# Kernel optimization log

Hardware: AMD Instinct MI355X
Metric: run time of the kernel (lower is better)

The kernel has to match this reference:

```python
import jax, jax.numpy as jnp
import numpy as np

B = 512
N_DRUGS = 4096
H_DRUG = 1023          # per-drug feature dim; input to MLP is 2*(H_DRUG+1) = 2048
N_CELL = 32
DIMS = [2048, 2048, 1024, 512, 1]


def setup_inputs() -> dict:
    key = jax.random.key(0)
    ks = jax.random.split(key, 12)
    pairs = jax.random.randint(ks[0], (B, 2), 0, N_DRUGS)
    cell_lines = jax.random.randint(ks[1], (B,), 0, N_CELL)
    attrs = jax.random.normal(ks[2], (B, 4), dtype=jnp.float32)
    h_drug = jax.random.normal(ks[3], (N_DRUGS, H_DRUG), dtype=jnp.float32)
    # shared Linear layers (torch Linear: y = x @ W.T + b), kaiming-uniform-ish init
    def lin(k, fan_in, fan_out):
        k1, k2 = jax.random.split(k)
        bound = 1.0 / np.sqrt(fan_in)
        W = jax.random.uniform(k1, (fan_out, fan_in), jnp.float32, -bound, bound)
        b = jax.random.uniform(k2, (fan_out,), jnp.float32, -bound, bound)
        return W, b
    W0, b0 = lin(ks[4], DIMS[0], DIMS[1])
    W1, b1 = lin(ks[5], DIMS[1], DIMS[2])
    # cell-line specific layers: 1/100 * randn
    L0 = 0.01 * jax.random.normal(ks[6], (N_CELL, DIMS[3], DIMS[2]), dtype=jnp.float32)
    O0 = 0.01 * jax.random.normal(ks[7], (N_CELL, DIMS[3], 1), dtype=jnp.float32)
    L1 = 0.01 * jax.random.normal(ks[8], (N_CELL, DIMS[4], DIMS[3]), dtype=jnp.float32)
    O1 = 0.01 * jax.random.normal(ks[9], (N_CELL, DIMS[4], 1), dtype=jnp.float32)
    return {"pairs": pairs, "cell_lines": cell_lines, "attrs": attrs, "h_drug": h_drug,
            "W0": W0, "b0": b0, "W1": W1, "b1": b1,
            "L0": L0, "O0": O0, "L1": L1, "O1": O1}


def reference(pairs, cell_lines, attrs, h_drug, W0, b0, W1, b1, L0, O0, L1, O1):
    n_attr = attrs.shape[1] // 2
    h1 = h_drug[pairs[:, 0]]                               # [B, H_DRUG]
    h2 = h_drug[pairs[:, 1]]
    bd1 = jnp.concatenate([h1, attrs[:, n_attr - 1:n_attr]], axis=1)
    bd2 = jnp.concatenate([h2, attrs[:, -1:]], axis=1)
    # original flips order with p=0.5 (data augmentation); fixed to (bd1, bd2) for determinism
    x = jnp.concatenate([bd1, bd2], axis=1)                # [B, 2048]
    # shared MLP (note: original applies relu(relu(x)) == relu(x))
    x = jax.nn.relu(x @ W0.T + b0)                         # [B, 2048]
    x = jax.nn.relu(x @ W1.T + b1)                         # [B, 1024]
    # cell-line-specific layers: gather per-sample weight and batched matvec
    x = jax.nn.relu(jnp.einsum('boi,bi->bo', L0[cell_lines], x) + O0[cell_lines, :, 0])  # [B, 512]
    x = jnp.einsum('boi,bi->bo', L1[cell_lines], x) + O1[cell_lines, :, 0]               # [B, 1]
    return x[:, 0]
```

## Files before the change

kernel.cpp:

```cpp
#include <hip/hip_runtime.h>

typedef short s16x8 __attribute__((ext_vector_type(8)));
typedef float f32x4 __attribute__((ext_vector_type(4)));
typedef unsigned short u16;

#define BATCH 512
#define HD    1023
#define K0    2048
#define N0    2048
#define N1    1024
#define N2    512

__device__ __forceinline__ u16 f2bf(float f) {
  unsigned u = __builtin_bit_cast(unsigned, f);
  unsigned r = (u + 0x7fffu + ((u >> 16) & 1u)) >> 16;
  return (u16)r;
}

__device__ __forceinline__ s16x8 pack8(f32x4 a, f32x4 b) {
  union { unsigned u[4]; s16x8 v; } r;
  asm("v_cvt_pk_bf16_f32 %0, %1, %2" : "=v"(r.u[0]) : "v"(a[0]), "v"(a[1]));
  asm("v_cvt_pk_bf16_f32 %0, %1, %2" : "=v"(r.u[1]) : "v"(a[2]), "v"(a[3]));
  asm("v_cvt_pk_bf16_f32 %0, %1, %2" : "=v"(r.u[2]) : "v"(b[0]), "v"(b[1]));
  asm("v_cvt_pk_bf16_f32 %0, %1, %2" : "=v"(r.u[3]) : "v"(b[2]), "v"(b[3]));
  return r.v;
}

__global__ __launch_bounds__(256) void k_prep(
    const int* __restrict__ pairs, const float* __restrict__ attrs,
    const float* __restrict__ h_drug, const float* __restrict__ W0,
    const float* __restrict__ W1, const int* __restrict__ cells,
    const float* __restrict__ O1, u16* __restrict__ xb,
    u16* __restrict__ w0b, u16* __restrict__ w1b, float* __restrict__ out) {
  const int bid = blockIdx.x, tid = threadIdx.x;
  if (bid < 512) {
    const int b = bid;
    const float* h0 = h_drug + (size_t)pairs[2 * b] * HD;
    const float* h1 = h_drug + (size_t)pairs[2 * b + 1] * HD;
    u16* xr = xb + (size_t)b * K0;
    for (int i = tid; i < HD; i += 256) {
      xr[i] = f2bf(h0[i]);
      xr[1024 + i] = f2bf(h1[i]);
    }
    if (tid == 0) {
      xr[1023] = f2bf(attrs[4 * b + 1]);
      xr[2047] = f2bf(attrs[4 * b + 3]);
      out[b] = O1[cells[b]];
    }
  } else if (bid < 1536) {
    const size_t e = ((size_t)(bid - 512) * 256 + tid) * 16;
    f32x4 a = *(const f32x4*)(W0 + e),     b2 = *(const f32x4*)(W0 + e + 4);
    f32x4 c = *(const f32x4*)(W0 + e + 8), d  = *(const f32x4*)(W0 + e + 12);
    *(s16x8*)(w0b + e)     = pack8(a, b2);
    *(s16x8*)(w0b + e + 8) = pack8(c, d);
  } else {
    const size_t e = ((size_t)(bid - 1536) * 256 + tid) * 16;
    f32x4 a = *(const f32x4*)(W1 + e),     b2 = *(const f32x4*)(W1 + e + 4);
    f32x4 c = *(const f32x4*)(W1 + e + 8), d  = *(const f32x4*)(W1 + e + 12);
    *(s16x8*)(w1b + e)     = pack8(a, b2);
    *(s16x8*)(w1b + e + 8) = pack8(c, d);
  }
}

#define GI(s, t) { \
  pa0_##s = *(const s16x8*)(agp0 + (size_t)(t) * 128); \
  if constexpr (AF == 2) pa1_##s = *(const s16x8*)(agp1 + (size_t)(t) * 128); \
  pb_##s = *(const s16x8*)(bgp0 + (size_t)(t) * 128); }

#define GS(s, t, DOLOAD) { \
  char* buf = lds[(s) & 1]; \
  *(s16x8*)(buf + awo0) = pa0_##s; \
  if constexpr (AF == 2) *(s16x8*)(buf + awo1) = pa1_##s; \
  *(s16x8*)(buf + ABYTES + bwo0) = pb_##s; \
  asm volatile("s_waitcnt lgkmcnt(0)" ::: "memory"); \
  __builtin_amdgcn_s_barrier(); \
  asm volatile("" ::: "memory"); \
  if (DOLOAD) GI(s, (t) + 4) \
  __builtin_amdgcn_s_setprio(1); \
  _Pragma("unroll") \
  for (int ks = 0; ks < 2; ++ks) { \
    const int kq = ((ks << 6) | lk) ^ sw; \
    s16x8 a0 = *(const s16x8*)(buf + aoff + kq); \
    s16x8 b0 = *(const s16x8*)(buf + ABYTES + boff + kq); \
    acc0 = __builtin_amdgcn_mfma_f32_16x16x32_bf16(a0, b0, acc0, 0, 0, 0); \
    if constexpr (AF == 2) { \
      s16x8 a1 = *(const s16x8*)(buf + aoff + 2048 + kq); \
      acc1 = __builtin_amdgcn_mfma_f32_16x16x32_bf16(a1, b0, acc1, 0, 0, 0); \
    } \
  } \
  __builtin_amdgcn_s_setprio(0); }

template <int BM, int N>
__global__ __launch_bounds__(256) void k_gemm(
    const u16* __restrict__ A, const u16* __restrict__ B,
    const float* __restrict__ bias, u16* __restrict__ Y) {
  constexpr int K = 2048;
  constexpr int AF = BM / 32;
  constexpr int ABYTES = BM * 128;
  constexpr int NBMSH = (BM == 64) ? 3 : 4;
  __shared__ char lds[2][ABYTES + 4096];
  const int tid = threadIdx.x;
  const int w = tid >> 6, l = tid & 63;
  const int wr = w >> 1, wc = w & 1;
  const int lrow = l & 15;
  const int lk = (l >> 4) << 4;
  const int sw = (lrow & 7) << 4;

  const int wgid = (blockIdx.x & 7) * 64 + (blockIdx.x >> 3);
  const int bn = wgid >> NBMSH, bm = wgid & ((1 << NBMSH) - 1);

  const size_t K2 = (size_t)K * 2;
  const char* Ag = (const char*)A + (size_t)bm * BM * K2;
  const char* Bg = (const char*)B + (size_t)(bn * 32) * K2;

  const int o0 = tid * 16;
  const int ar0 = o0 >> 7, ac0 = o0 & 127;
  const char* agp0 = Ag + (size_t)ar0 * K2 + ac0;
  const int awo0 = (ar0 << 7) + (ac0 ^ ((ar0 & 7) << 4));
  const int o1 = o0 + 4096;
  const int ar1 = o1 >> 7, ac1 = o1 & 127;
  const char* agp1 = Ag + (size_t)ar1 * K2 + ac1;
  const int awo1 = (ar1 << 7) + (ac1 ^ ((ar1 & 7) << 4));

  const char* bgp0 = Bg + (size_t)ar0 * K2 + ac0;
  const int bwo0 = awo0;

  const int aoff = (wr * (BM / 2) + lrow) * 128;
  const int boff = (wc * 16 + lrow) * 128;

  f32x4 acc0 = {}, acc1 = {};
  s16x8 pa0_0, pa0_1, pa0_2, pa0_3;
  s16x8 pa1_0, pa1_1, pa1_2, pa1_3;
  s16x8 pb_0, pb_1, pb_2, pb_3;

  GI(0, 0) GI(1, 1) GI(2, 2) GI(3, 3)
  constexpr int NT = 32;
  int t = 0;
  for (; t < NT - 4; t += 4) {
    GS(0, t, 1) GS(1, t + 1, 1) GS(2, t + 2, 1) GS(3, t + 3, 1)
  }
  GS(0, t, 0) GS(1, t + 1, 0) GS(2, t + 2, 0) GS(3, t + 3, 0)

  const int colg = bn * 32 + wc * 16 + lrow;
  const int rowb = bm * BM + wr * (BM / 2) + ((l >> 4) << 2);
  const float bv = bias[colg];
#pragma unroll
  for (int fa = 0; fa < AF; ++fa)
#pragma unroll
    for (int r = 0; r < 4; ++r) {
      float v = (fa ? acc1 : acc0)[r] + bv;
      v = v > 0.f ? v : 0.f;
      Y[(size_t)(rowb + fa * 16 + r) * N + colg] = f2bf(v);
    }
}

#define H_ISSUE(S, ch) { \
  const float* src = hsrc + (ch) * 256; \
  q0_##S = *(const f32x4*)(src);      q1_##S = *(const f32x4*)(src + 4); \
  q2_##S = *(const f32x4*)(src + 8);  q3_##S = *(const f32x4*)(src + 12); \
  q4_##S = *(const f32x4*)(src + 16); q5_##S = *(const f32x4*)(src + 20); \
  q6_##S = *(const f32x4*)(src + 24); q7_##S = *(const f32x4*)(src + 28); }

#define H_WRITE(S, ch) { \
  char* dst = lbuf[(ch) & 1] + (hrow << 9); \
  *(s16x8*)(dst + ((hcb + 0)  ^ hswz)) = pack8(q0_##S, q1_##S); \
  *(s16x8*)(dst + ((hcb + 16) ^ hswz)) = pack8(q2_##S, q3_##S); \
  *(s16x8*)(dst + ((hcb + 32) ^ hswz)) = pack8(q4_##S, q5_##S); \
  *(s16x8*)(dst + ((hcb + 48) ^ hswz)) = pack8(q6_##S, q7_##S); }

#define H_SYNC { \
  asm volatile("s_waitcnt lgkmcnt(0)" ::: "memory"); \
  __builtin_amdgcn_s_barrier(); \
  asm volatile("" ::: "memory"); }

#define H_MFMA(ch) { \
  const char* bb = lbuf[(ch) & 1]; \
  s16x8 bv0 = *(const s16x8*)(bb + ((0 * 16 + lrow) << 9) + kboff); \
  s16x8 bv1 = *(const s16x8*)(bb + ((1 * 16 + lrow) << 9) + kboff); \
  s16x8 bv2 = *(const s16x8*)(bb + ((2 * 16 + lrow) << 9) + kboff); \
  s16x8 bv3 = *(const s16x8*)(bb + ((3 * 16 + lrow) << 9) + kboff); \
  s16x8 av0 = *(const s16x8*)(ap0 + (ch) * 256); \
  s16x8 av1 = *(const s16x8*)(ap1 + (ch) * 256); \
  __builtin_amdgcn_s_setprio(1); \
  acc[0][0] = __builtin_amdgcn_mfma_f32_16x16x32_bf16(av0, bv0, acc[0][0], 0, 0, 0); \
  acc[0][1] = __builtin_amdgcn_mfma_f32_16x16x32_bf16(av0, bv1, acc[0][1], 0, 0, 0); \
  acc[0][2] = __builtin_amdgcn_mfma_f32_16x16x32_bf16(av0, bv2, acc[0][2], 0, 0, 0); \
  acc[0][3] = __builtin_amdgcn_mfma_f32_16x16x32_bf16(av0, bv3, acc[0][3], 0, 0, 0); \
  acc[1][0] = __builtin_amdgcn_mfma_f32_16x16x32_bf16(av1, bv0, acc[1][0], 0, 0, 0); \
  acc[1][1] = __builtin_amdgcn_mfma_f32_16x16x32_bf16(av1, bv1, acc[1][1], 0, 0, 0); \
  acc[1][2] = __builtin_amdgcn_mfma_f32_16x16x32_bf16(av1, bv2, acc[1][2], 0, 0, 0); \
  acc[1][3] = __builtin_amdgcn_mfma_f32_16x16x32_bf16(av1, bv3, acc[1][3], 0, 0, 0); \
  __builtin_amdgcn_s_setprio(0); }

__global__ __launch_bounds__(512) void k_head(
    const int* __restrict__ cells, const u16* __restrict__ y2b,
    const float* __restrict__ L0, const float* __restrict__ O0,
    const float* __restrict__ L1, float* __restrict__ out) {
  __shared__ int slist[544];
  __shared__ int scnt;
  __shared__ float red[8][2048];
  __shared__ char lbuf[2][32768];
  const int tid = threadIdx.x;
  const int c = blockIdx.x >> 3, rt = blockIdx.x & 7;
  if (tid == 0) scnt = 0;
  __syncthreads();
  for (int i = tid; i < BATCH; i += 512)
    if (cells[i] == c) slist[atomicAdd(&scnt, 1)] = i;
  __syncthreads();
  const int ns = scnt;
  if (ns == 0) return;
  const int npad = (ns + 31) & ~31;
  for (int i = ns + tid; i < npad; i += 512) slist[i] = slist[0];
  __syncthreads();

  const int w = tid >> 6, l = tid & 63;
  const int lrow = l & 15;
  const int r0 = rt * 64;
  const float* L0c = L0 + ((size_t)c * N2 + r0) * N1;
  const int hrow = tid >> 3;
  const int hcb = (tid & 7) * 64;
  const int hswz = (hrow & 7) << 4;
  const float* hsrc = L0c + (size_t)hrow * N1 + (tid & 7) * 32;
  const int kboff = ((w * 64 + ((l >> 4) << 4)) ^ ((lrow & 7) << 4));

  f32x4 q0_A, q1_A, q2_A, q3_A, q4_A, q5_A, q6_A, q7_A;
  f32x4 q0_B, q1_B, q2_B, q3_B, q4_B, q5_B, q6_B, q7_B;

  for (int cb = 0; cb < npad; cb += 32) {
    const u16* ap0 = y2b + (size_t)slist[cb + lrow] * N1 + w * 32 + ((l >> 4) << 3);
    const u16* ap1 = y2b + (size_t)slist[cb + 16 + lrow] * N1 + w * 32 + ((l >> 4) << 3);
    f32x4 acc[2][4] = {};
    H_ISSUE(A, 0)
    H_WRITE(A, 0)
    H_ISSUE(B, 1)
    H_SYNC
    H_MFMA(0)
    H_WRITE(B, 1)
    H_ISSUE(A, 2)
    H_SYNC
    H_MFMA(1)
    H_WRITE(A, 2)
    H_ISSUE(B, 3)
    H_SYNC
    H_MFMA(2)
    H_WRITE(B, 3)
    H_SYNC
    H_MFMA(3)

    __syncthreads();
#pragma unroll
    for (int h = 0; h < 2; ++h)
#pragma unroll
      for (int fb = 0; fb < 4; ++fb)
#pragma unroll
        for (int r = 0; r < 4; ++r) {
          const int s0 = h * 16 + (l >> 4) * 4 + r;
          red[w][s0 * 64 + fb * 16 + lrow] = acc[h][fb][r];
        }
    __syncthreads();
    {
      const int s = tid >> 4;
      const int rq = (tid & 15) * 4;
      if (cb + s < ns) {
        float p = 0.f;
#pragma unroll
        for (int j = 0; j < 4; ++j) {
          const int r = rq + j, e = s * 64 + r;
          float v = red[0][e] + red[1][e] + red[2][e] + red[3][e] +
                    red[4][e] + red[5][e] + red[6][e] + red[7][e] +
                    O0[(size_t)c * N2 + r0 + r];
          v = v > 0.f ? v : 0.f;
          p += v * L1[(size_t)c * N2 + r0 + r];
        }
#pragma unroll
        for (int off = 8; off; off >>= 1) p += __shfl_xor(p, off, 16);
        if ((tid & 15) == 0) atomicAdd(&out[slist[cb + s]], p);
      }
    }
  }
}

extern "C" void kernel_launch(void* const* d_in, const int* in_sizes, int n_in,
                              void* d_out, int out_size, void* d_ws, size_t ws_size,
                              hipStream_t stream) {
  const int*   pairs  = (const int*)d_in[0];
  const int*   cells  = (const int*)d_in[1];
  const float* attrs  = (const float*)d_in[2];
  const float* h_drug = (const float*)d_in[3];
  const float* W0     = (const float*)d_in[4];
  const float* b0     = (const float*)d_in[5];
  const float* W1     = (const float*)d_in[6];
  const float* b1     = (const float*)d_in[7];
  const float* L0     = (const float*)d_in[8];
  const float* O0     = (const float*)d_in[9];
  const float* L1     = (const float*)d_in[10];
  const float* O1     = (const float*)d_in[11];
  float* out = (float*)d_out;

  char* ws = (char*)d_ws;
  u16* xb  = (u16*)(ws);
  u16* w0b = (u16*)(ws + (2u  << 20));
  u16* w1b = (u16*)(ws + (10u << 20));
  u16* y1b = (u16*)(ws + (14u << 20));
  u16* y2b = (u16*)(ws + (16u << 20));

  k_prep<<<2048, 256, 0, stream>>>(pairs, attrs, h_drug, W0, W1, cells, O1,
                                   xb, w0b, w1b, out);
  k_gemm<64, N0><<<512, 256, 0, stream>>>(xb, w0b, b0, y1b);
  k_gemm<32, N1><<<512, 256, 0, stream>>>(y1b, w1b, b1, y2b);
  k_head<<<256, 512, 0, stream>>>(cells, y2b, L0, O0, L1, out);
}
```

Measured before the change: 48.26 us.

## Move W1 bf16 conversion into first GEMM launch and enlarge its tiles

New measurement: 46.22 us. 4.2% less time.

```diff
diff --git a/kernel.cpp b/kernel.cpp
--- a/kernel.cpp
+++ b/kernel.cpp
@@ -29,9 +29,8 @@
 __global__ __launch_bounds__(256) void k_prep(
     const int* __restrict__ pairs, const float* __restrict__ attrs,
     const float* __restrict__ h_drug, const float* __restrict__ W0,
-    const float* __restrict__ W1, const int* __restrict__ cells,
-    const float* __restrict__ O1, u16* __restrict__ xb,
-    u16* __restrict__ w0b, u16* __restrict__ w1b, float* __restrict__ out) {
+    const int* __restrict__ cells, const float* __restrict__ O1,
+    u16* __restrict__ xb, u16* __restrict__ w0b, float* __restrict__ out) {
   const int bid = blockIdx.x, tid = threadIdx.x;
   if (bid < 512) {
     const int b = bid;
@@ -47,31 +46,107 @@
       xr[2047] = f2bf(attrs[4 * b + 3]);
       out[b] = O1[cells[b]];
     }
-  } else if (bid < 1536) {
+  } else {
     const size_t e = ((size_t)(bid - 512) * 256 + tid) * 16;
     f32x4 a = *(const f32x4*)(W0 + e),     b2 = *(const f32x4*)(W0 + e + 4);
     f32x4 c = *(const f32x4*)(W0 + e + 8), d  = *(const f32x4*)(W0 + e + 12);
     *(s16x8*)(w0b + e)     = pack8(a, b2);
     *(s16x8*)(w0b + e + 8) = pack8(c, d);
-  } else {
-    const size_t e = ((size_t)(bid - 1536) * 256 + tid) * 16;
-    f32x4 a = *(const f32x4*)(W1 + e),     b2 = *(const f32x4*)(W1 + e + 4);
-    f32x4 c = *(const f32x4*)(W1 + e + 8), d  = *(const f32x4*)(W1 + e + 12);
-    *(s16x8*)(w1b + e)     = pack8(a, b2);
-    *(s16x8*)(w1b + e + 8) = pack8(c, d);
-  }
+  }
+}
+
+#define GI1(s, t) { \
+  pa_##s = *(const s16x8*)(agp0 + (size_t)(t) * 128); \
+  pb_##s = *(const s16x8*)(bgp0 + (size_t)(t) * 128); }
+
+#define GS1(s, t, DOLOAD) { \
+  char* buf = lds[(s) & 1]; \
+  *(s16x8*)(buf + awo0) = pa_##s; \
+  *(s16x8*)(buf + 8192 + awo0) = pb_##s; \
+  asm volatile("s_waitcnt lgkmcnt(0)" ::: "memory"); \
+  __builtin_amdgcn_s_barrier(); \
+  asm volatile("" ::: "memory"); \
+  if (DOLOAD) GI1(s, (t) + 4) \
+  __builtin_amdgcn_s_setprio(1); \
+  _Pragma("unroll") \
+  for (int ks = 0; ks < 2; ++ks) { \
+    const int kq = ((ks << 6) | lk) ^ sw; \
+    s16x8 a0 = *(const s16x8*)(buf + aoff + kq); \
+    s16x8 a1 = *(const s16x8*)(buf + aoff + 2048 + kq); \
+    s16x8 b0 = *(const s16x8*)(buf + 8192 + boff + kq); \
+    acc0 = __builtin_amdgcn_mfma_f32_16x16x32_bf16(a0, b0, acc0, 0, 0, 0); \
+    acc1 = __builtin_amdgcn_mfma_f32_16x16x32_bf16(a1, b0, acc1, 0, 0, 0); \
+  } \
+  __builtin_amdgcn_s_setprio(0); }
+
+__global__ __launch_bounds__(512) void k_gemm1(
+    const u16* __restrict__ A, const u16* __restrict__ B,
+    const float* __restrict__ bias, u16* __restrict__ Y,
+    const float* __restrict__ W1f, u16* __restrict__ w1b) {
+  constexpr int K = 2048, N = 2048;
+  if (blockIdx.x >= 256) {
+    const size_t e = (((size_t)blockIdx.x - 256) * 512 + threadIdx.x) * 8;
+    f32x4 a = *(const f32x4*)(W1f + e), b2 = *(const f32x4*)(W1f + e + 4);
+    *(s16x8*)(w1b + e) = pack8(a, b2);
+    return;
+  }
+  __shared__ char lds[2][16384];
+  const int tid = threadIdx.x;
+  const int w = tid >> 6, l = tid & 63;
+  const int wr = w >> 2, wn = w & 3;
+  const int lrow = l & 15;
+  const int lk = (l >> 4) << 4;
+  const int sw = (lrow & 7) << 4;
+
+  const int wgid = (blockIdx.x & 7) * 32 + (blockIdx.x >> 3);
+  const int bn = wgid >> 3, bm = wgid & 7;
+
+  const size_t K2 = (size_t)K * 2;
+  const char* Ag = (const char*)A + (size_t)bm * 64 * K2;
+  const char* Bg = (const char*)B + (size_t)bn * 64 * K2;
+
+  const int o0 = tid * 16;
+  const int ar0 = o0 >> 7, ac0 = o0 & 127;
+  const char* agp0 = Ag + (size_t)ar0 * K2 + ac0;
+  const char* bgp0 = Bg + (size_t)ar0 * K2 + ac0;
+  const int awo0 = (ar0 << 7) + (ac0 ^ ((ar0 & 7) << 4));
+
+  const int aoff = (wr * 32 + lrow) * 128;
+  const int boff = (wn * 16 + lrow) * 128;
+
+  f32x4 acc0 = {}, acc1 = {};
+  s16x8 pa_0, pa_1, pa_2, pa_3;
+  s16x8 pb_0, pb_1, pb_2, pb_3;
+
+  GI1(0, 0) GI1(1, 1) GI1(2, 2) GI1(3, 3)
+  constexpr int NT = 32;
+  int t = 0;
+  for (; t < NT - 4; t += 4) {
+    GS1(0, t, 1) GS1(1, t + 1, 1) GS1(2, t + 2, 1) GS1(3, t + 3, 1)
+  }
+  GS1(0, t, 0) GS1(1, t + 1, 0) GS1(2, t + 2, 0) GS1(3, t + 3, 0)
+
+  const int colg = bn * 64 + wn * 16 + lrow;
+  const int rowb = bm * 64 + wr * 32 + ((l >> 4) << 2);
+  const float bv = bias[colg];
+#pragma unroll
+  for (int fa = 0; fa < 2; ++fa)
+#pragma unroll
+    for (int r = 0; r < 4; ++r) {
+      float v = (fa ? acc1 : acc0)[r] + bv;
+      v = v > 0.f ? v : 0.f;
+      Y[(size_t)(rowb + fa * 16 + r) * N + colg] = f2bf(v);
+    }
 }
 
 #define GI(s, t) { \
   pa0_##s = *(const s16x8*)(agp0 + (size_t)(t) * 128); \
-  if constexpr (AF == 2) pa1_##s = *(const s16x8*)(agp1 + (size_t)(t) * 128); \
   pb_##s = *(const s16x8*)(bgp0 + (size_t)(t) * 128); }
 
 #define GS(s, t, DOLOAD) { \
   char* buf = lds[(s) & 1]; \
   *(s16x8*)(buf + awo0) = pa0_##s; \
-  if constexpr (AF == 2) *(s16x8*)(buf + awo1) = pa1_##s; \
-  *(s16x8*)(buf + ABYTES + bwo0) = pb_##s; \
+  *(s16x8*)(buf + ABYTES + awo0) = pb_##s; \
   asm volatile("s_waitcnt lgkmcnt(0)" ::: "memory"); \
   __builtin_amdgcn_s_barrier(); \
   asm volatile("" ::: "memory"); \
@@ -83,21 +158,14 @@
     s16x8 a0 = *(const s16x8*)(buf + aoff + kq); \
     s16x8 b0 = *(const s16x8*)(buf + ABYTES + boff + kq); \
     acc0 = __builtin_amdgcn_mfma_f32_16x16x32_bf16(a0, b0, acc0, 0, 0, 0); \
-    if constexpr (AF == 2) { \
-      s16x8 a1 = *(const s16x8*)(buf + aoff + 2048 + kq); \
-      acc1 = __builtin_amdgcn_mfma_f32_16x16x32_bf16(a1, b0, acc1, 0, 0, 0); \
-    } \
   } \
   __builtin_amdgcn_s_setprio(0); }
 
-template <int BM, int N>
-__global__ __launch_bounds__(256) void k_gemm(
+__global__ __launch_bounds__(256) void k_gemm2(
     const u16* __restrict__ A, const u16* __restrict__ B,
     const float* __restrict__ bias, u16* __restrict__ Y) {
-  constexpr int K = 2048;
-  constexpr int AF = BM / 32;
-  constexpr int ABYTES = BM * 128;
-  constexpr int NBMSH = (BM == 64) ? 3 : 4;
+  constexpr int K = 2048, N = 1024;
+  constexpr int ABYTES = 32 * 128;
   __shared__ char lds[2][ABYTES + 4096];
   const int tid = threadIdx.x;
   const int w = tid >> 6, l = tid & 63;
@@ -107,30 +175,23 @@
   const int sw = (lrow & 7) << 4;
 
   const int wgid = (blockIdx.x & 7) * 64 + (blockIdx.x >> 3);
-  const int bn = wgid >> NBMSH, bm = wgid & ((1 << NBMSH) - 1);
+  const int bn = wgid >> 4, bm = wgid & 15;
 
   const size_t K2 = (size_t)K * 2;
-  const char* Ag = (const char*)A + (size_t)bm * BM * K2;
+  const char* Ag = (const char*)A + (size_t)bm * 32 * K2;
   const char* Bg = (const char*)B + (size_t)(bn * 32) * K2;
 
   const int o0 = tid * 16;
   const int ar0 = o0 >> 7, ac0 = o0 & 127;
   const char* agp0 = Ag + (size_t)ar0 * K2 + ac0;
+  const char* bgp0 = Bg + (size_t)ar0 * K2 + ac0;
   const int awo0 = (ar0 << 7) + (ac0 ^ ((ar0 & 7) << 4));
-  const int o1 = o0 + 4096;
-  const int ar1 = o1 >> 7, ac1 = o1 & 127;
-  const char* agp1 = Ag + (size_t)ar1 * K2 + ac1;
-  const int awo1 = (ar1 << 7) + (ac1 ^ ((ar1 & 7) << 4));
-
-  const char* bgp0 = Bg + (size_t)ar0 * K2 + ac0;
-  const int bwo0 = awo0;
-
-  const int aoff = (wr * (BM / 2) + lrow) * 128;
+
+  const int aoff = (wr * 16 + lrow) * 128;
   const int boff = (wc * 16 + lrow) * 128;
 
-  f32x4 acc0 = {}, acc1 = {};
+  f32x4 acc0 = {};
   s16x8 pa0_0, pa0_1, pa0_2, pa0_3;
-  s16x8 pa1_0, pa1_1, pa1_2, pa1_3;
   s16x8 pb_0, pb_1, pb_2, pb_3;
 
   GI(0, 0) GI(1, 1) GI(2, 2) GI(3, 3)
@@ -142,16 +203,14 @@
   GS(0, t, 0) GS(1, t + 1, 0) GS(2, t + 2, 0) GS(3, t + 3, 0)
 
   const int colg = bn * 32 + wc * 16 + lrow;
-  const int rowb = bm * BM + wr * (BM / 2) + ((l >> 4) << 2);
+  const int rowb = bm * 32 + wr * 16 + ((l >> 4) << 2);
   const float bv = bias[colg];
 #pragma unroll
-  for (int fa = 0; fa < AF; ++fa)
-#pragma unroll
-    for (int r = 0; r < 4; ++r) {
-      float v = (fa ? acc1 : acc0)[r] + bv;
-      v = v > 0.f ? v : 0.f;
-      Y[(size_t)(rowb + fa * 16 + r) * N + colg] = f2bf(v);
-    }
+  for (int r = 0; r < 4; ++r) {
+    float v = acc0[r] + bv;
+    v = v > 0.f ? v : 0.f;
+    Y[(size_t)(rowb + r) * N + colg] = f2bf(v);
+  }
 }
 
 #define H_ISSUE(S, ch) { \
@@ -304,9 +363,9 @@
   u16* y1b = (u16*)(ws + (14u << 20));
   u16* y2b = (u16*)(ws + (16u << 20));
 
-  k_prep<<<2048, 256, 0, stream>>>(pairs, attrs, h_drug, W0, W1, cells, O1,
-                                   xb, w0b, w1b, out);
-  k_gemm<64, N0><<<512, 256, 0, stream>>>(xb, w0b, b0, y1b);
-  k_gemm<32, N1><<<512, 256, 0, stream>>>(y1b, w1b, b1, y2b);
+  k_prep<<<1536, 256, 0, stream>>>(pairs, attrs, h_drug, W0, cells, O1,
+                                   xb, w0b, out);
+  k_gemm1<<<768, 512, 0, stream>>>(xb, w0b, b0, y1b, W1, w1b);
+  k_gemm2<<<512, 256, 0, stream>>>(y1b, w1b, b1, y2b);
   k_head<<<256, 512, 0, stream>>>(cells, y2b, L0, O0, L1, out);
 }
```
